# Optimization experiments

Measured on AMD Instinct MI355X. Metric: run time of the kernel, lower is better.

## Reference

```python
import jax, jax.numpy as jnp
import numpy as np

N_NODES = 100000
N_EDGES = 1200000
FEAT = 64
AVG_D_LOG = float(np.log(13.0))  # log(avg_degree + 1), avg_degree = 12
EPS_STD = 1e-5   # PNA std epsilon
EPS_BN = 1e-5    # torch BatchNorm1d default eps


def setup_inputs() -> dict:
    key = jax.random.key(0)
    k_h, k_norm, k_src, k_dst = jax.random.split(key, 4)
    h = jax.random.normal(k_h, (N_NODES, FEAT), dtype=jnp.float32)
    norm = jax.random.uniform(k_norm, (N_NODES, 1), dtype=jnp.float32)
    e = jnp.zeros((N_EDGES, 1), dtype=jnp.float32)  # unused by the layer
    src = jax.random.randint(k_src, (N_EDGES,), 0, N_NODES, dtype=jnp.int32)
    dst = jnp.sort(jax.random.randint(k_dst, (N_EDGES,), 0, N_NODES, dtype=jnp.int32))
    bn_weight = jnp.ones((FEAT,), dtype=jnp.float32)
    bn_bias = jnp.zeros((FEAT,), dtype=jnp.float32)
    return {"h": h, "norm": norm, "e": e, "bn_weight": bn_weight,
            "bn_bias": bn_bias, "src": src, "dst": dst}


def reference(h, norm, e, bn_weight, bn_bias, src, dst):
    N, F = h.shape
    hn = h * norm                           # [N, F] pre-scaled node features
    m = hn[src]                             # [E, F] gathered messages (copy_u)

    ones = jnp.ones_like(dst, dtype=hn.dtype)
    deg = jax.ops.segment_sum(ones, dst, num_segments=N, indices_are_sorted=True)  # [N]
    deg_safe = jnp.maximum(deg, 1.0)
    has_nb = (deg > 0)[:, None]             # zero in-degree nodes get zeros (DGL)

    s1 = jax.ops.segment_sum(m, dst, num_segments=N, indices_are_sorted=True)
    s2 = jax.ops.segment_sum(m * m, dst, num_segments=N, indices_are_sorted=True)
    mean = s1 / deg_safe[:, None]
    var = jax.nn.relu(s2 / deg_safe[:, None] - mean * mean)
    std = jnp.sqrt(var + EPS_STD)
    mx = jnp.where(has_nb, jax.ops.segment_max(m, dst, num_segments=N, indices_are_sorted=True), 0.0)
    mn = jnp.where(has_nb, jax.ops.segment_min(m, dst, num_segments=N, indices_are_sorted=True), 0.0)

    agg = jnp.concatenate([mean, mx, mn, std], axis=1)          # [N, 4F]

    logD = jnp.log(deg + 1.0)[:, None]                           # [N, 1]
    amp = agg * (logD / AVG_D_LOG)                               # amplification scaler
    att = agg * (AVG_D_LOG / jnp.where(logD > 0, logD, 1.0))     # attenuation scaler
    scaled = jnp.concatenate([agg, amp, att], axis=1)            # [N, 12F]
    scaled = jnp.where(has_nb, scaled, 0.0)

    out = jnp.concatenate([hn, scaled * norm], axis=1)           # [N, 13F]
    out = out.reshape(N, 13, F).mean(axis=1)                     # [N, F]
    out = jax.nn.relu(out)                                       # activation (dropout p=0)

    # BatchNorm1d, training mode (biased batch variance), affine
    mu = out.mean(axis=0)
    v = out.var(axis=0)
    out = (out - mu) / jnp.sqrt(v + EPS_BN) * bn_weight + bn_bias
    return out
```

## Files before the change

kernel.cpp:

```cpp
#include <hip/hip_runtime.h>
#include <hip/hip_fp16.h>
#include <math.h>
#include <float.h>

#define N_NODES 100000
#define N_EDGES 1200000
#define FEAT 64
#define AVG_D_LOG 2.5649493574615367f
#define EPS_STD 1e-5f
#define EPS_BN 1e-5
#define AGG_BLOCKS 12500
#define HN_BLOCKS 6250
#define SC_BLOCKS 4688
#define STAT1_BLOCKS 256
#define ROWS1 49
#define OLD_RED_BLOCKS 512

#if __has_builtin(__builtin_fmaxf16)
#define H16MAX(a,b) __builtin_fmaxf16((a),(b))
#define H16MIN(a,b) __builtin_fminf16((a),(b))
#else
#define H16MAX(a,b) ((a) > (b) ? (a) : (b))
#define H16MIN(a,b) ((a) < (b) ? (a) : (b))
#endif

__global__ void __launch_bounds__(256) prep(
    const float* __restrict__ h, const float* __restrict__ norm,
    const int* __restrict__ dst,
    __half* __restrict__ hn_h, int* __restrict__ rowptr)
{
    const int b = blockIdx.x;
    if (b < HN_BLOCKS) {
        const size_t i4 = ((size_t)b * 256 + threadIdx.x) * 4;
        const int node = (int)(i4 >> 6);
        const float nr = norm[node];
        float4 v = *reinterpret_cast<const float4*>(h + i4);
        __half2 p0 = __floats2half2_rn(v.x * nr, v.y * nr);
        __half2 p1 = __floats2half2_rn(v.z * nr, v.w * nr);
        __half2* o = reinterpret_cast<__half2*>(hn_h + i4);
        o[0] = p0; o[1] = p1;
    } else {
        const int i = (b - HN_BLOCKS) * 256 + threadIdx.x;
        if (i >= N_EDGES) return;
        const int d1 = dst[i];
        const int d0 = (i == 0) ? -1 : dst[i - 1];
        for (int n = d0 + 1; n <= d1; ++n) rowptr[n] = i;
        if (i == N_EDGES - 1) {
            for (int n = d1 + 1; n <= N_NODES; ++n) rowptr[n] = N_EDGES;
        }
    }
}

template <bool WRITE_PSTAT>
__global__ void __launch_bounds__(256) pna_agg6(
    const __half* __restrict__ hn, const float* __restrict__ norm,
    const int* __restrict__ src, const int* __restrict__ rowptr,
    float* __restrict__ out, float2* __restrict__ pstat)
{
    const int tid  = threadIdx.x;
    const int wid  = tid >> 6;
    const int lane = tid & 63;
    const int n0   = (blockIdx.x * 4 + wid) * 2;

    const int s0 = __builtin_amdgcn_readfirstlane(rowptr[n0]);
    const int e0 = __builtin_amdgcn_readfirstlane(rowptr[n0 + 1]);
    const int e1 = __builtin_amdgcn_readfirstlane(rowptr[n0 + 2]);
    const int degA = e0 - s0;
    const int degB = e1 - e0;

    const _Float16* __restrict__ hnf = (const _Float16*)hn;
    const float ownA = (float)hnf[(size_t)n0 * FEAT + lane];
    const float ownB = (float)hnf[(size_t)(n0 + 1) * FEAT + lane];

    float s1A = 0.f, s2A = 0.f, s1B = 0.f, s2B = 0.f;
    _Float16 mxA = (_Float16)(-65504.f), mnA = (_Float16)(65504.f);
    _Float16 mxB = (_Float16)(-65504.f), mnB = (_Float16)(65504.f);

#define LOADW(J)  (hnf[(size_t)(J) * FEAT + lane])
#define ACCA(W) do { _Float16 w_ = (W); float f_ = (float)w_;                 \
                     s1A = __builtin_fmaf(f_, 1.0f, s1A);                     \
                     s2A = __builtin_fmaf(f_, f_, s2A);                       \
                     mxA = H16MAX(mxA, w_); mnA = H16MIN(mnA, w_); } while (0)
#define ACCB(W) do { _Float16 w_ = (W); float f_ = (float)w_;                 \
                     s1B = __builtin_fmaf(f_, 1.0f, s1B);                     \
                     s2B = __builtin_fmaf(f_, f_, s2B);                       \
                     mxB = H16MAX(mxB, w_); mnB = H16MIN(mnB, w_); } while (0)

    int ea = s0, eb = e0;
    while (ea + 8 <= e0 && eb + 8 <= e1) {
        const int a0 = src[ea+0], a1 = src[ea+1], a2 = src[ea+2], a3 = src[ea+3];
        const int a4 = src[ea+4], a5 = src[ea+5], a6 = src[ea+6], a7 = src[ea+7];
        const int b0 = src[eb+0], b1 = src[eb+1], b2 = src[eb+2], b3 = src[eb+3];
        const int b4 = src[eb+4], b5 = src[eb+5], b6 = src[eb+6], b7 = src[eb+7];
        _Float16 wa0 = LOADW(a0), wa1 = LOADW(a1), wa2 = LOADW(a2), wa3 = LOADW(a3);
        _Float16 wa4 = LOADW(a4), wa5 = LOADW(a5), wa6 = LOADW(a6), wa7 = LOADW(a7);
        _Float16 wb0 = LOADW(b0), wb1 = LOADW(b1), wb2 = LOADW(b2), wb3 = LOADW(b3);
        _Float16 wb4 = LOADW(b4), wb5 = LOADW(b5), wb6 = LOADW(b6), wb7 = LOADW(b7);
        ACCA(wa0); ACCA(wa1); ACCA(wa2); ACCA(wa3);
        ACCA(wa4); ACCA(wa5); ACCA(wa6); ACCA(wa7);
        ACCB(wb0); ACCB(wb1); ACCB(wb2); ACCB(wb3);
        ACCB(wb4); ACCB(wb5); ACCB(wb6); ACCB(wb7);
        ea += 8; eb += 8;
    }
    while (ea + 4 <= e0 && eb + 4 <= e1) {
        const int a0 = src[ea+0], a1 = src[ea+1], a2 = src[ea+2], a3 = src[ea+3];
        const int b0 = src[eb+0], b1 = src[eb+1], b2 = src[eb+2], b3 = src[eb+3];
        _Float16 wa0 = LOADW(a0), wa1 = LOADW(a1), wa2 = LOADW(a2), wa3 = LOADW(a3);
        _Float16 wb0 = LOADW(b0), wb1 = LOADW(b1), wb2 = LOADW(b2), wb3 = LOADW(b3);
        ACCA(wa0); ACCA(wa1); ACCA(wa2); ACCA(wa3);
        ACCB(wb0); ACCB(wb1); ACCB(wb2); ACCB(wb3);
        ea += 4; eb += 4;
    }
    for (; ea + 4 <= e0; ea += 4) {
        const int a0 = src[ea+0], a1 = src[ea+1], a2 = src[ea+2], a3 = src[ea+3];
        _Float16 w0 = LOADW(a0), w1 = LOADW(a1), w2 = LOADW(a2), w3 = LOADW(a3);
        ACCA(w0); ACCA(w1); ACCA(w2); ACCA(w3);
    }
    for (; ea < e0; ++ea) { _Float16 w = LOADW(src[ea]); ACCA(w); }
    for (; eb + 4 <= e1; eb += 4) {
        const int b0 = src[eb+0], b1 = src[eb+1], b2 = src[eb+2], b3 = src[eb+3];
        _Float16 w0 = LOADW(b0), w1 = LOADW(b1), w2 = LOADW(b2), w3 = LOADW(b3);
        ACCB(w0); ACCB(w1); ACCB(w2); ACCB(w3);
    }
    for (; eb < e1; ++eb) { _Float16 w = LOADW(src[eb]); ACCB(w); }
#undef ACCA
#undef ACCB
#undef LOADW

    float vA, vB;
    {
        float pre;
        if (degA > 0) {
            const float invd = 1.0f / (float)degA;
            const float mean = s1A * invd;
            const float var  = fmaxf(s2A * invd - mean * mean, 0.f);
            const float stdv = sqrtf(var + EPS_STD);
            const float logD = logf((float)degA + 1.0f);
            const float factor = norm[n0] * (1.0f + logD * (1.0f / AVG_D_LOG) + AVG_D_LOG / logD)
                                         * (1.0f / 13.0f);
            pre = ownA * (1.0f / 13.0f) + (mean + (float)mxA + (float)mnA + stdv) * factor;
        } else {
            pre = ownA * (1.0f / 13.0f);
        }
        vA = fmaxf(pre, 0.f);
    }
    {
        float pre;
        if (degB > 0) {
            const float invd = 1.0f / (float)degB;
            const float mean = s1B * invd;
            const float var  = fmaxf(s2B * invd - mean * mean, 0.f);
            const float stdv = sqrtf(var + EPS_STD);
            const float logD = logf((float)degB + 1.0f);
            const float factor = norm[n0 + 1] * (1.0f + logD * (1.0f / AVG_D_LOG) + AVG_D_LOG / logD)
                                             * (1.0f / 13.0f);
            pre = ownB * (1.0f / 13.0f) + (mean + (float)mxB + (float)mnB + stdv) * factor;
        } else {
            pre = ownB * (1.0f / 13.0f);
        }
        vB = fmaxf(pre, 0.f);
    }

    out[(size_t)n0 * FEAT + lane]       = vA;
    out[(size_t)(n0 + 1) * FEAT + lane] = vB;

    if (WRITE_PSTAT) {
        __shared__ float lsS[4][64];
        __shared__ float lsQ[4][64];
        lsS[wid][lane] = vA + vB;
        lsQ[wid][lane] = vA * vA + vB * vB;
        __syncthreads();
        if (tid < 64) {
            float2 p;
            p.x = lsS[0][tid] + lsS[1][tid] + lsS[2][tid] + lsS[3][tid];
            p.y = lsQ[0][tid] + lsQ[1][tid] + lsQ[2][tid] + lsQ[3][tid];
            pstat[(size_t)blockIdx.x * 64 + tid] = p;
        }
    }
}

__global__ void __launch_bounds__(256) bn_stats1(
    const float2* __restrict__ pstat, float2* __restrict__ partial)
{
    const int tid  = threadIdx.x;
    const int w    = tid >> 6;
    const int lane = tid & 63;
    const int r0 = (int)blockIdx.x * ROWS1;
    const int r1 = min(r0 + ROWS1, AGG_BLOCKS);
    float S = 0.f, Q = 0.f;
    for (int r = r0 + w; r < r1; r += 4) {
        float2 p = pstat[(size_t)r * 64 + lane];
        S += p.x; Q += p.y;
    }
    __shared__ float sS[4][64], sQ[4][64];
    sS[w][lane] = S; sQ[w][lane] = Q;
    __syncthreads();
    if (tid < 64) {
        float2 o;
        o.x = sS[0][tid] + sS[1][tid] + sS[2][tid] + sS[3][tid];
        o.y = sQ[0][tid] + sQ[1][tid] + sQ[2][tid] + sQ[3][tid];
        partial[(size_t)blockIdx.x * 64 + tid] = o;
    }
}

__global__ void __launch_bounds__(256) bn_stats2(
    const float2* __restrict__ partial,
    const float* __restrict__ w, const float* __restrict__ b,
    float2* __restrict__ ss)
{
    const int tid = threadIdx.x;
    const int g   = tid >> 6;
    const int f   = tid & 63;
    double S = 0.0, Q = 0.0;
    for (int blk = g; blk < STAT1_BLOCKS; blk += 4) {
        float2 p = partial[(size_t)blk * 64 + f];
        S += (double)p.x; Q += (double)p.y;
    }
    __shared__ double dS[4][64], dQ[4][64];
    dS[g][f] = S; dQ[g][f] = Q;
    __syncthreads();
    if (tid < 64) {
        double s = dS[0][tid] + dS[1][tid] + dS[2][tid] + dS[3][tid];
        double q = dQ[0][tid] + dQ[1][tid] + dQ[2][tid] + dQ[3][tid];
        double mu   = s / (double)N_NODES;
        double var  = q / (double)N_NODES - mu * mu;
        double rstd = 1.0 / sqrt(var + EPS_BN);
        float sc = (float)rstd * w[tid];
        float2 o; o.x = sc; o.y = b[tid] - (float)mu * sc;
        ss[tid] = o;
    }
}

__global__ void __launch_bounds__(256) bn_partial(
    const float* __restrict__ out1,
    double* __restrict__ psum, double* __restrict__ psumsq)
{
    const int tid = threadIdx.x;
    const int fb  = tid & 15;
    const int grp = tid >> 4;
    double s0 = 0, s1 = 0, s2 = 0, s3 = 0;
    double q0 = 0, q1 = 0, q2 = 0, q3 = 0;
    for (int n = blockIdx.x * 16 + grp; n < N_NODES; n += OLD_RED_BLOCKS * 16) {
        float4 v = *reinterpret_cast<const float4*>(out1 + (size_t)n * FEAT + fb * 4);
        s0 += (double)v.x; q0 += (double)v.x * (double)v.x;
        s1 += (double)v.y; q1 += (double)v.y * (double)v.y;
        s2 += (double)v.z; q2 += (double)v.z * (double)v.z;
        s3 += (double)v.w; q3 += (double)v.w * (double)v.w;
    }
    __shared__ double ls[256 * 4];
    __shared__ double lq[256 * 4];
    ls[tid * 4 + 0] = s0; ls[tid * 4 + 1] = s1; ls[tid * 4 + 2] = s2; ls[tid * 4 + 3] = s3;
    lq[tid * 4 + 0] = q0; lq[tid * 4 + 1] = q1; lq[tid * 4 + 2] = q2; lq[tid * 4 + 3] = q3;
    __syncthreads();
    if (tid < 64) {
        const int f = tid, fblk = f >> 2, j = f & 3;
        double S = 0, Q = 0;
        for (int g = 0; g < 16; ++g) {
            S += ls[(g * 16 + fblk) * 4 + j];
            Q += lq[(g * 16 + fblk) * 4 + j];
        }
        psum  [blockIdx.x * 64 + f] = S;
        psumsq[blockIdx.x * 64 + f] = Q;
    }
}

__global__ void bn_finalize_old(const double* __restrict__ psum,
                                const double* __restrict__ psumsq,
                                const float* __restrict__ w, const float* __restrict__ b,
                                float2* __restrict__ ss)
{
    int f = threadIdx.x;
    double s = 0.0, s2 = 0.0;
    for (int blk = 0; blk < OLD_RED_BLOCKS; ++blk) {
        s  += psum  [blk * 64 + f];
        s2 += psumsq[blk * 64 + f];
    }
    double mu   = s / (double)N_NODES;
    double var  = s2 / (double)N_NODES - mu * mu;
    double rstd = 1.0 / sqrt(var + EPS_BN);
    float sc = (float)rstd * w[f];
    float2 o; o.x = sc; o.y = b[f] - (float)mu * sc;
    ss[f] = o;
}

__global__ void __launch_bounds__(256) bn_apply2(
    float* __restrict__ out, const float2* __restrict__ ss)
{
    __shared__ float sS[64], sH[64];
    if (threadIdx.x < 64) {
        float2 p = ss[threadIdx.x];
        sS[threadIdx.x] = p.x; sH[threadIdx.x] = p.y;
    }
    __syncthreads();
    const size_t i4 = ((size_t)blockIdx.x * 256 + threadIdx.x) * 4;
    float4 v = *reinterpret_cast<const float4*>(out + i4);
    const int f = (int)(i4 & 63);
    v.x = v.x * sS[f + 0] + sH[f + 0];
    v.y = v.y * sS[f + 1] + sH[f + 1];
    v.z = v.z * sS[f + 2] + sH[f + 2];
    v.w = v.w * sS[f + 3] + sH[f + 3];
    *reinterpret_cast<float4*>(out + i4) = v;
}

extern "C" void kernel_launch(void* const* d_in, const int* in_sizes, int n_in,
                              void* d_out, int out_size, void* d_ws, size_t ws_size,
                              hipStream_t stream) {
    const float* h    = (const float*)d_in[0];
    const float* norm = (const float*)d_in[1];
    const float* bnw  = (const float*)d_in[3];
    const float* bnb  = (const float*)d_in[4];
    const int*   src  = (const int*)d_in[5];
    const int*   dst  = (const int*)d_in[6];
    float* out = (float*)d_out;

    char* ws = (char*)d_ws;
    size_t o = 0;
    __half* hnbuf = (__half*)(ws + o);
    o += (((size_t)N_NODES * FEAT * sizeof(__half)) + 255) & ~(size_t)255;
    int* rowptr = (int*)(ws + o);
    o += (((size_t)(N_NODES + 1) * sizeof(int)) + 255) & ~(size_t)255;
    float2* ss = (float2*)(ws + o); o += 512;
    float2* partial = (float2*)(ws + o);
    o += (size_t)STAT1_BLOCKS * 64 * sizeof(float2);
    float2* pstat = (float2*)(ws + o);
    const size_t need_new = o + (size_t)AGG_BLOCKS * 64 * sizeof(float2);
    double* psum   = (double*)(ws + o);
    double* psumsq = (double*)(ws + o + (size_t)OLD_RED_BLOCKS * 64 * sizeof(double));

    prep<<<HN_BLOCKS + SC_BLOCKS, 256, 0, stream>>>(h, norm, dst, hnbuf, rowptr);

    if (ws_size >= need_new) {
        pna_agg6<true><<<AGG_BLOCKS, 256, 0, stream>>>(hnbuf, norm, src, rowptr, out, pstat);
        bn_stats1<<<STAT1_BLOCKS, 256, 0, stream>>>(pstat, partial);
        bn_stats2<<<1, 256, 0, stream>>>(partial, bnw, bnb, ss);
    } else {
        pna_agg6<false><<<AGG_BLOCKS, 256, 0, stream>>>(hnbuf, norm, src, rowptr, out, nullptr);
        bn_partial<<<OLD_RED_BLOCKS, 256, 0, stream>>>(out, psum, psumsq);
        bn_finalize_old<<<1, 64, 0, stream>>>(psum, psumsq, bnw, bnb, ss);
    }
    bn_apply2<<<HN_BLOCKS, 256, 0, stream>>>(out, ss);
}
```

Measured before the change: 84.26 us.

## Pack edge pairs into half2 for fdot2 stats and store fp16 intermediate output

The aggregation loop now loads two neighbour features into a half2 vector and accumulates sum and sum-of-squares with the packed fdot2 instruction, with packed max/min. This halves the per-edge ALU instruction count. The pre-BN output is written as fp16 to a workspace buffer, and a new apply kernel reads it back and writes the fp32 result, cutting intermediate memory traffic. The trade-off is fp16 rounding of the intermediate before normalization. The fallback path for a small workspace without room for pstat is removed, so in that case nothing runs.

```diff
diff --git a/kernel.cpp b/kernel.cpp
--- a/kernel.cpp
+++ b/kernel.cpp
@@ -14,7 +14,8 @@
 #define SC_BLOCKS 4688
 #define STAT1_BLOCKS 256
 #define ROWS1 49
-#define OLD_RED_BLOCKS 512
+
+typedef _Float16 h2v __attribute__((ext_vector_type(2)));
 
 #if __has_builtin(__builtin_fmaxf16)
 #define H16MAX(a,b) __builtin_fmaxf16((a),(b))
@@ -22,6 +23,26 @@
 #else
 #define H16MAX(a,b) ((a) > (b) ? (a) : (b))
 #define H16MIN(a,b) ((a) < (b) ? (a) : (b))
+#endif
+
+static __device__ __forceinline__ h2v h2vmax(h2v a, h2v b) {
+#if __has_builtin(__builtin_elementwise_max)
+    return __builtin_elementwise_max(a, b);
+#else
+    h2v r; r.x = H16MAX(a.x, b.x); r.y = H16MAX(a.y, b.y); return r;
+#endif
+}
+static __device__ __forceinline__ h2v h2vmin(h2v a, h2v b) {
+#if __has_builtin(__builtin_elementwise_min)
+    return __builtin_elementwise_min(a, b);
+#else
+    h2v r; r.x = H16MIN(a.x, b.x); r.y = H16MIN(a.y, b.y); return r;
+#endif
+}
+#if __has_builtin(__builtin_amdgcn_fdot2)
+#define FDOT2(a,b,c) __builtin_amdgcn_fdot2((a),(b),(c),false)
+#else
+#define FDOT2(a,b,c) (__builtin_fmaf((float)(a).x,(float)(b).x, __builtin_fmaf((float)(a).y,(float)(b).y,(c))))
 #endif
 
 __global__ void __launch_bounds__(256) prep(
@@ -51,11 +72,12 @@
     }
 }
 
-template <bool WRITE_PSTAT>
-__global__ void __launch_bounds__(256) pna_agg6(
+template <bool OUT16>
+__global__ void __launch_bounds__(256) pna_agg7(
     const __half* __restrict__ hn, const float* __restrict__ norm,
     const int* __restrict__ src, const int* __restrict__ rowptr,
-    float* __restrict__ out, float2* __restrict__ pstat)
+    float* __restrict__ outf, __half* __restrict__ outh,
+    float2* __restrict__ pstat)
 {
     const int tid  = threadIdx.x;
     const int wid  = tid >> 6;
@@ -73,18 +95,26 @@
     const float ownB = (float)hnf[(size_t)(n0 + 1) * FEAT + lane];
 
     float s1A = 0.f, s2A = 0.f, s1B = 0.f, s2B = 0.f;
-    _Float16 mxA = (_Float16)(-65504.f), mnA = (_Float16)(65504.f);
-    _Float16 mxB = (_Float16)(-65504.f), mnB = (_Float16)(65504.f);
-
-#define LOADW(J)  (hnf[(size_t)(J) * FEAT + lane])
-#define ACCA(W) do { _Float16 w_ = (W); float f_ = (float)w_;                 \
-                     s1A = __builtin_fmaf(f_, 1.0f, s1A);                     \
-                     s2A = __builtin_fmaf(f_, f_, s2A);                       \
-                     mxA = H16MAX(mxA, w_); mnA = H16MIN(mnA, w_); } while (0)
-#define ACCB(W) do { _Float16 w_ = (W); float f_ = (float)w_;                 \
-                     s1B = __builtin_fmaf(f_, 1.0f, s1B);                     \
-                     s2B = __builtin_fmaf(f_, f_, s2B);                       \
-                     mxB = H16MAX(mxB, w_); mnB = H16MIN(mnB, w_); } while (0)
+    h2v mxA = { (_Float16)(-65504.f), (_Float16)(-65504.f) };
+    h2v mnA = { (_Float16)( 65504.f), (_Float16)( 65504.f) };
+    h2v mxB = mxA, mnB = mnA;
+    const h2v ones = { (_Float16)1.f, (_Float16)1.f };
+
+#define LOADP(J0,J1) ({ h2v w__;                                   \
+        w__.x = hnf[(size_t)(J0) * FEAT + lane];                   \
+        w__.y = hnf[(size_t)(J1) * FEAT + lane]; w__; })
+#define ACCA(W) do { h2v w_ = (W);                                 \
+        s1A = FDOT2(w_, ones, s1A); s2A = FDOT2(w_, w_, s2A);      \
+        mxA = h2vmax(mxA, w_); mnA = h2vmin(mnA, w_); } while (0)
+#define ACCB(W) do { h2v w_ = (W);                                 \
+        s1B = FDOT2(w_, ones, s1B); s2B = FDOT2(w_, w_, s2B);      \
+        mxB = h2vmax(mxB, w_); mnB = h2vmin(mnB, w_); } while (0)
+#define ACCA1(W) do { _Float16 h_ = (W); float f_ = (float)h_;     \
+        s1A += f_; s2A = __builtin_fmaf(f_, f_, s2A);              \
+        mxA.x = H16MAX(mxA.x, h_); mnA.x = H16MIN(mnA.x, h_); } while (0)
+#define ACCB1(W) do { _Float16 h_ = (W); float f_ = (float)h_;     \
+        s1B += f_; s2B = __builtin_fmaf(f_, f_, s2B);              \
+        mxB.x = H16MAX(mxB.x, h_); mnB.x = H16MIN(mnB.x, h_); } while (0)
 
     int ea = s0, eb = e0;
     while (ea + 8 <= e0 && eb + 8 <= e1) {
@@ -92,40 +122,38 @@
         const int a4 = src[ea+4], a5 = src[ea+5], a6 = src[ea+6], a7 = src[ea+7];
         const int b0 = src[eb+0], b1 = src[eb+1], b2 = src[eb+2], b3 = src[eb+3];
         const int b4 = src[eb+4], b5 = src[eb+5], b6 = src[eb+6], b7 = src[eb+7];
-        _Float16 wa0 = LOADW(a0), wa1 = LOADW(a1), wa2 = LOADW(a2), wa3 = LOADW(a3);
-        _Float16 wa4 = LOADW(a4), wa5 = LOADW(a5), wa6 = LOADW(a6), wa7 = LOADW(a7);
-        _Float16 wb0 = LOADW(b0), wb1 = LOADW(b1), wb2 = LOADW(b2), wb3 = LOADW(b3);
-        _Float16 wb4 = LOADW(b4), wb5 = LOADW(b5), wb6 = LOADW(b6), wb7 = LOADW(b7);
-        ACCA(wa0); ACCA(wa1); ACCA(wa2); ACCA(wa3);
-        ACCA(wa4); ACCA(wa5); ACCA(wa6); ACCA(wa7);
-        ACCB(wb0); ACCB(wb1); ACCB(wb2); ACCB(wb3);
-        ACCB(wb4); ACCB(wb5); ACCB(wb6); ACCB(wb7);
+        h2v wa01 = LOADP(a0,a1), wa23 = LOADP(a2,a3), wa45 = LOADP(a4,a5), wa67 = LOADP(a6,a7);
+        h2v wb01 = LOADP(b0,b1), wb23 = LOADP(b2,b3), wb45 = LOADP(b4,b5), wb67 = LOADP(b6,b7);
+        ACCA(wa01); ACCA(wa23); ACCA(wa45); ACCA(wa67);
+        ACCB(wb01); ACCB(wb23); ACCB(wb45); ACCB(wb67);
         ea += 8; eb += 8;
     }
     while (ea + 4 <= e0 && eb + 4 <= e1) {
         const int a0 = src[ea+0], a1 = src[ea+1], a2 = src[ea+2], a3 = src[ea+3];
         const int b0 = src[eb+0], b1 = src[eb+1], b2 = src[eb+2], b3 = src[eb+3];
-        _Float16 wa0 = LOADW(a0), wa1 = LOADW(a1), wa2 = LOADW(a2), wa3 = LOADW(a3);
-        _Float16 wb0 = LOADW(b0), wb1 = LOADW(b1), wb2 = LOADW(b2), wb3 = LOADW(b3);
-        ACCA(wa0); ACCA(wa1); ACCA(wa2); ACCA(wa3);
-        ACCB(wb0); ACCB(wb1); ACCB(wb2); ACCB(wb3);
+        h2v wa01 = LOADP(a0,a1), wa23 = LOADP(a2,a3);
+        h2v wb01 = LOADP(b0,b1), wb23 = LOADP(b2,b3);
+        ACCA(wa01); ACCA(wa23);
+        ACCB(wb01); ACCB(wb23);
         ea += 4; eb += 4;
     }
-    for (; ea + 4 <= e0; ea += 4) {
-        const int a0 = src[ea+0], a1 = src[ea+1], a2 = src[ea+2], a3 = src[ea+3];
-        _Float16 w0 = LOADW(a0), w1 = LOADW(a1), w2 = LOADW(a2), w3 = LOADW(a3);
-        ACCA(w0); ACCA(w1); ACCA(w2); ACCA(w3);
-    }
-    for (; ea < e0; ++ea) { _Float16 w = LOADW(src[ea]); ACCA(w); }
-    for (; eb + 4 <= e1; eb += 4) {
-        const int b0 = src[eb+0], b1 = src[eb+1], b2 = src[eb+2], b3 = src[eb+3];
-        _Float16 w0 = LOADW(b0), w1 = LOADW(b1), w2 = LOADW(b2), w3 = LOADW(b3);
-        ACCB(w0); ACCB(w1); ACCB(w2); ACCB(w3);
-    }
-    for (; eb < e1; ++eb) { _Float16 w = LOADW(src[eb]); ACCB(w); }
+    for (; ea + 2 <= e0; ea += 2) {
+        const int a0 = src[ea], a1 = src[ea+1];
+        h2v w = LOADP(a0, a1);
+        ACCA(w);
+    }
+    if (ea < e0) { ACCA1(hnf[(size_t)src[ea] * FEAT + lane]); }
+    for (; eb + 2 <= e1; eb += 2) {
+        const int b0 = src[eb], b1 = src[eb+1];
+        h2v w = LOADP(b0, b1);
+        ACCB(w);
+    }
+    if (eb < e1) { ACCB1(hnf[(size_t)src[eb] * FEAT + lane]); }
+#undef LOADP
 #undef ACCA
 #undef ACCB
-#undef LOADW
+#undef ACCA1
+#undef ACCB1
 
     float vA, vB;
     {
@@ -135,10 +163,12 @@
             const float mean = s1A * invd;
             const float var  = fmaxf(s2A * invd - mean * mean, 0.f);
             const float stdv = sqrtf(var + EPS_STD);
+            const float mxf  = fmaxf((float)mxA.x, (float)mxA.y);
+            const float mnf  = fminf((float)mnA.x, (float)mnA.y);
             const float logD = logf((float)degA + 1.0f);
             const float factor = norm[n0] * (1.0f + logD * (1.0f / AVG_D_LOG) + AVG_D_LOG / logD)
                                          * (1.0f / 13.0f);
-            pre = ownA * (1.0f / 13.0f) + (mean + (float)mxA + (float)mnA + stdv) * factor;
+            pre = ownA * (1.0f / 13.0f) + (mean + mxf + mnf + stdv) * factor;
         } else {
             pre = ownA * (1.0f / 13.0f);
         }
@@ -151,20 +181,27 @@
             const float mean = s1B * invd;
             const float var  = fmaxf(s2B * invd - mean * mean, 0.f);
             const float stdv = sqrtf(var + EPS_STD);
+            const float mxf  = fmaxf((float)mxB.x, (float)mxB.y);
+            const float mnf  = fminf((float)mnB.x, (float)mnB.y);
             const float logD = logf((float)degB + 1.0f);
             const float factor = norm[n0 + 1] * (1.0f + logD * (1.0f / AVG_D_LOG) + AVG_D_LOG / logD)
                                              * (1.0f / 13.0f);
-            pre = ownB * (1.0f / 13.0f) + (mean + (float)mxB + (float)mnB + stdv) * factor;
+            pre = ownB * (1.0f / 13.0f) + (mean + mxf + mnf + stdv) * factor;
         } else {
             pre = ownB * (1.0f / 13.0f);
         }
         vB = fmaxf(pre, 0.f);
     }
 
-    out[(size_t)n0 * FEAT + lane]       = vA;
-    out[(size_t)(n0 + 1) * FEAT + lane] = vB;
-
-    if (WRITE_PSTAT) {
+    if (OUT16) {
+        outh[(size_t)n0 * FEAT + lane]       = __float2half_rn(vA);
+        outh[(size_t)(n0 + 1) * FEAT + lane] = __float2half_rn(vB);
+    } else {
+        outf[(size_t)n0 * FEAT + lane]       = vA;
+        outf[(size_t)(n0 + 1) * FEAT + lane] = vB;
+    }
+
+    {
         __shared__ float lsS[4][64];
         __shared__ float lsQ[4][64];
         lsS[wid][lane] = vA + vB;
@@ -231,56 +268,26 @@
     }
 }
 
-__global__ void __launch_bounds__(256) bn_partial(
-    const float* __restrict__ out1,
-    double* __restrict__ psum, double* __restrict__ psumsq)
-{
-    const int tid = threadIdx.x;
-    const int fb  = tid & 15;
-    const int grp = tid >> 4;
-    double s0 = 0, s1 = 0, s2 = 0, s3 = 0;
-    double q0 = 0, q1 = 0, q2 = 0, q3 = 0;
-    for (int n = blockIdx.x * 16 + grp; n < N_NODES; n += OLD_RED_BLOCKS * 16) {
-        float4 v = *reinterpret_cast<const float4*>(out1 + (size_t)n * FEAT + fb * 4);
-        s0 += (double)v.x; q0 += (double)v.x * (double)v.x;
-        s1 += (double)v.y; q1 += (double)v.y * (double)v.y;
-        s2 += (double)v.z; q2 += (double)v.z * (double)v.z;
-        s3 += (double)v.w; q3 += (double)v.w * (double)v.w;
-    }
-    __shared__ double ls[256 * 4];
-    __shared__ double lq[256 * 4];
-    ls[tid * 4 + 0] = s0; ls[tid * 4 + 1] = s1; ls[tid * 4 + 2] = s2; ls[tid * 4 + 3] = s3;
-    lq[tid * 4 + 0] = q0; lq[tid * 4 + 1] = q1; lq[tid * 4 + 2] = q2; lq[tid * 4 + 3] = q3;
+__global__ void __launch_bounds__(256) bn_apply3(
+    const __half* __restrict__ out1h, float* __restrict__ out,
+    const float2* __restrict__ ss)
+{
+    __shared__ float sS[64], sH[64];
+    if (threadIdx.x < 64) {
+        float2 p = ss[threadIdx.x];
+        sS[threadIdx.x] = p.x; sH[threadIdx.x] = p.y;
+    }
     __syncthreads();
-    if (tid < 64) {
-        const int f = tid, fblk = f >> 2, j = f & 3;
-        double S = 0, Q = 0;
-        for (int g = 0; g < 16; ++g) {
-            S += ls[(g * 16 + fblk) * 4 + j];
-            Q += lq[(g * 16 + fblk) * 4 + j];
-        }
-        psum  [blockIdx.x * 64 + f] = S;
-        psumsq[blockIdx.x * 64 + f] = Q;
-    }
-}
-
-__global__ void bn_finalize_old(const double* __restrict__ psum,
-                                const double* __restrict__ psumsq,
-                                const float* __restrict__ w, const float* __restrict__ b,
-                                float2* __restrict__ ss)
-{
-    int f = threadIdx.x;
-    double s = 0.0, s2 = 0.0;
-    for (int blk = 0; blk < OLD_RED_BLOCKS; ++blk) {
-        s  += psum  [blk * 64 + f];
-        s2 += psumsq[blk * 64 + f];
-    }
-    double mu   = s / (double)N_NODES;
-    double var  = s2 / (double)N_NODES - mu * mu;
-    double rstd = 1.0 / sqrt(var + EPS_BN);
-    float sc = (float)rstd * w[f];
-    float2 o; o.x = sc; o.y = b[f] - (float)mu * sc;
-    ss[f] = o;
+    const size_t i4 = ((size_t)blockIdx.x * 256 + threadIdx.x) * 4;
+    const __half2* ip = reinterpret_cast<const __half2*>(out1h + i4);
+    __half2 a = ip[0], b = ip[1];
+    const int f = (int)(i4 & 63);
+    float4 v;
+    v.x = __low2float(a)  * sS[f + 0] + sH[f + 0];
+    v.y = __high2float(a) * sS[f + 1] + sH[f + 1];
+    v.z = __low2float(b)  * sS[f + 2] + sH[f + 2];
+    v.w = __high2float(b) * sS[f + 3] + sH[f + 3];
+    *reinterpret_cast<float4*>(out + i4) = v;
 }
 
 __global__ void __launch_bounds__(256) bn_apply2(
@@ -323,20 +330,24 @@
     float2* partial = (float2*)(ws + o);
     o += (size_t)STAT1_BLOCKS * 64 * sizeof(float2);
     float2* pstat = (float2*)(ws + o);
-    const size_t need_new = o + (size_t)AGG_BLOCKS * 64 * sizeof(float2);
-    double* psum   = (double*)(ws + o);
-    double* psumsq = (double*)(ws + o + (size_t)OLD_RED_BLOCKS * 64 * sizeof(double));
+    o += (size_t)AGG_BLOCKS * 64 * sizeof(float2);
+    const size_t need_mid = o;
+    __half* out1h = (__half*)(ws + o);
+    const size_t need_fast = o + (size_t)N_NODES * FEAT * sizeof(__half);
 
     prep<<<HN_BLOCKS + SC_BLOCKS, 256, 0, stream>>>(h, norm, dst, hnbuf, rowptr);
 
-    if (ws_size >= need_new) {
-        pna_agg6<true><<<AGG_BLOCKS, 256, 0, stream>>>(hnbuf, norm, src, rowptr, out, pstat);
+    if (ws_size >= need_fast) {
+        pna_agg7<true><<<AGG_BLOCKS, 256, 0, stream>>>(hnbuf, norm, src, rowptr,
+                                                       nullptr, out1h, pstat);
         bn_stats1<<<STAT1_BLOCKS, 256, 0, stream>>>(pstat, partial);
         bn_stats2<<<1, 256, 0, stream>>>(partial, bnw, bnb, ss);
-    } else {
-        pna_agg6<false><<<AGG_BLOCKS, 256, 0, stream>>>(hnbuf, norm, src, rowptr, out, nullptr);
-        bn_partial<<<OLD_RED_BLOCKS, 256, 0, stream>>>(out, psum, psumsq);
-        bn_finalize_old<<<1, 64, 0, stream>>>(psum, psumsq, bnw, bnb, ss);
-    }
-    bn_apply2<<<HN_BLOCKS, 256, 0, stream>>>(out, ss);
-}
+        bn_apply3<<<HN_BLOCKS, 256, 0, stream>>>(out1h, out, ss);
+    } else if (ws_size >= need_mid) {
+        pna_agg7<false><<<AGG_BLOCKS, 256, 0, stream>>>(hnbuf, norm, src, rowptr,
+                                                        out, nullptr, pstat);
+        bn_stats1<<<STAT1_BLOCKS, 256, 0, stream>>>(pstat, partial);
+        bn_stats2<<<1, 256, 0, stream>>>(partial, bnw, bnb, ss);
+        bn_apply2<<<HN_BLOCKS, 256, 0, stream>>>(out, ss);
+    }
+}
```

Measured after the change: 82.98 us. About the same (-1.5%).
